# Kernel tuning notes

Hardware: AMD Instinct MI355X
Metric: run time of the kernel (lower is better)

## Reference

```python
import jax, jax.numpy as jnp
import numpy as np

MAX_DELTAS = 4  # number of concurrently loaded delta adapters


def _dequant(qw, qz, sc):
    """GPTQ-style 4-bit dequant with a single group (g_idx == 0).

    qw: [D, O, K//8] int32, 8 x 4-bit values packed along the input (K) dim.
    qz: [D, O//8, 1] int32, 8 x 4-bit zero points packed along the output dim.
    sc: [D, O, 1] float scales (one group).
    Returns dense delta weights [D, O, K].
    """
    shifts = jnp.arange(8, dtype=jnp.int32) * 4
    D, O, Kp = qw.shape
    w = ((qw[:, :, :, None] >> shifts) & 0xF).reshape(D, O, Kp * 8)   # [D,O,K]
    z = ((qz[:, :, 0][:, :, None] >> shifts) & 0xF).reshape(D, O)     # [D,O]
    return (w.astype(sc.dtype) - (z.astype(sc.dtype) + 1.0)[:, :, None]) * sc


def setup_inputs() -> dict:
    key = jax.random.key(0)
    ks = jax.random.split(key, 16)
    T, IN = 1024, 4096
    Q, KV = 4096, 1024  # 32 q-heads, 8 kv-heads, head_size 128
    OUT = Q + 2 * KV    # 6144
    D, PACK = MAX_DELTAS, 8
    IMAX = np.int32(2**31 - 1)
    return {
        "x": jax.random.normal(ks[0], (T, IN), dtype=jnp.float32),
        "w_base": jax.random.normal(ks[1], (OUT, IN), dtype=jnp.float32) * 0.02,
        "bias": jax.random.normal(ks[2], (OUT,), dtype=jnp.float32) * 0.02,
        "qweight_q": jax.random.randint(ks[3], (D, Q, IN // PACK), 0, IMAX, dtype=jnp.int32),
        "qweight_k": jax.random.randint(ks[4], (D, KV, IN // PACK), 0, IMAX, dtype=jnp.int32),
        "qweight_v": jax.random.randint(ks[5], (D, KV, IN // PACK), 0, IMAX, dtype=jnp.int32),
        "qzeros_q": jax.random.randint(ks[6], (D, Q // PACK, 1), 0, IMAX, dtype=jnp.int32),
        "qzeros_k": jax.random.randint(ks[7], (D, KV // PACK, 1), 0, IMAX, dtype=jnp.int32),
        "qzeros_v": jax.random.randint(ks[8], (D, KV // PACK, 1), 0, IMAX, dtype=jnp.int32),
        "scales_q": jax.random.uniform(ks[9], (D, Q, 1), dtype=jnp.float32) * 0.01,
        "scales_k": jax.random.uniform(ks[10], (D, KV, 1), dtype=jnp.float32) * 0.01,
        "scales_v": jax.random.uniform(ks[11], (D, KV, 1), dtype=jnp.float32) * 0.01,
        "indices": jax.random.randint(ks[12], (T,), 0, D, dtype=jnp.int32),
    }


def reference(x, w_base, bias, qweight_q, qweight_k, qweight_v,
              qzeros_q, qzeros_k, qzeros_v, scales_q, scales_k, scales_v,
              indices):
    # Base fused QKV projection.
    out = x @ w_base.T + bias  # [T, OUT]
    # Dequantize the three packed delta stacks and concatenate along out dim,
    # matching the (q, k, v) output_slices scatter of apply_delta.
    Wd = jnp.concatenate([
        _dequant(qweight_q, qzeros_q, scales_q),
        _dequant(qweight_k, qzeros_k, scales_k),
        _dequant(qweight_v, qzeros_v, scales_v),
    ], axis=1)  # [D, OUT, IN]
    # Per-token indexed delta matmul: token t uses adapter indices[t].
    for d in range(MAX_DELTAS):
        xm = jnp.where((indices == d)[:, None], x, 0.0)  # [T, IN]
        out = out + xm @ Wd[d].T
    return out
```

## Files before the change

### kernel.cpp

```cpp
#include <hip/hip_runtime.h>
#include <stdint.h>

#define T_TOK 1024
#define K_IN  4096
#define N_OUT 6144
#define N_Q   4096
#define N_KV  1024
#define N_D   4
#define KP    512

#define TM 128
#define TN 128
#define BK 64
#define NSTEPS (K_IN / BK)
#define PM_MAX 1536
#define MT (PM_MAX/TM)
#define NT (N_OUT/TN)
#define NBLK (NT * MT)

typedef __attribute__((ext_vector_type(8)))  short  short8;
typedef __attribute__((ext_vector_type(4)))  float  float4v;
typedef __attribute__((ext_vector_type(4)))  float  f32x4;
typedef __attribute__((ext_vector_type(4)))  uint   u32x4;

__device__ __forceinline__ ushort f2bf(float f) {
    uint32_t u = __float_as_uint(f);
    u = (u + 0x7FFFu + ((u >> 16) & 1u)) >> 16;
    return (ushort)u;
}
__device__ __forceinline__ uint pack2(ushort a, ushort b) {
    return (uint)a | ((uint)b << 16);
}

__device__ __forceinline__ short8 unpack_nib(uint q) {
    union { u32x4 u; short8 s; } r;
    uint t1 = q >> 8, t2 = q >> 16, t3 = q >> 24;
    r.u.x = ((q  & 0xFu) | ((q  & 0xF0u) << 12)) | 0x43004300u;
    r.u.y = ((t1 & 0xFu) | ((t1 & 0xF0u) << 12)) | 0x43004300u;
    r.u.z = ((t2 & 0xFu) | ((t2 & 0xF0u) << 12)) | 0x43004300u;
    r.u.w = ((t3 & 0xFu) | ((t3 & 0xF0u) << 12)) | 0x43004300u;
    return r.s;
}

__global__ void build_perm_kernel(const int* __restrict__ indices,
                                  int* __restrict__ perm,
                                  int* __restrict__ pofs) {
    int tid = threadIdx.x;
    for (int p = tid; p < PM_MAX; p += 256) perm[p] = -1;
    __syncthreads();
    if (tid >= 64) return;

    int cnt0 = 0, cnt1 = 0, cnt2 = 0, cnt3 = 0;
#pragma unroll
    for (int it = 0; it < T_TOK / 64; it++) {
        int d = indices[it * 64 + tid];
        cnt0 += __popcll(__ballot(d == 0));
        cnt1 += __popcll(__ballot(d == 1));
        cnt2 += __popcll(__ballot(d == 2));
        cnt3 += __popcll(__ballot(d == 3));
    }
    int cnt[4] = {cnt0, cnt1, cnt2, cnt3};
    int ps[5];
    int run = 0;
#pragma unroll
    for (int d = 0; d < N_D; d++) { ps[d] = run; run += ((cnt[d] + TM - 1) / TM) * TM; }
    ps[N_D] = run;
    if (tid == 0) {
#pragma unroll
        for (int d = 0; d <= N_D; d++) pofs[d] = ps[d];
    }
    unsigned long long ltmask = (tid == 63) ? 0x7FFFFFFFFFFFFFFFull
                                            : ((1ull << tid) - 1ull);
    int base[4] = {0, 0, 0, 0};
#pragma unroll
    for (int it = 0; it < T_TOK / 64; it++) {
        int d = indices[it * 64 + tid];
        unsigned long long m0 = __ballot(d == 0);
        unsigned long long m1 = __ballot(d == 1);
        unsigned long long m2 = __ballot(d == 2);
        unsigned long long m3 = __ballot(d == 3);
        unsigned long long md = (d == 0) ? m0 : (d == 1) ? m1 : (d == 2) ? m2 : m3;
        int rank = (int)__popcll(md & ltmask);
        int bse  = (d == 0) ? base[0] : (d == 1) ? base[1] : (d == 2) ? base[2] : base[3];
        int psd  = (d == 0) ? ps[0]   : (d == 1) ? ps[1]   : (d == 2) ? ps[2]   : ps[3];
        perm[psd + bse + rank] = it * 64 + tid;
        base[0] += __popcll(m0); base[1] += __popcll(m1);
        base[2] += __popcll(m2); base[3] += __popcll(m3);
    }
}

__global__ void wbconv_kernel(const float* __restrict__ w_base,
                              ushort* __restrict__ wb16) {
    int id = blockIdx.x * blockDim.x + threadIdx.x;
    const f32x4* src = (const f32x4*)(w_base + (size_t)id * 8);
    f32x4 a = __builtin_nontemporal_load(src);
    f32x4 b = __builtin_nontemporal_load(src + 1);
    u32x4 packv;
    packv.x = pack2(f2bf(a.x), f2bf(a.y));
    packv.y = pack2(f2bf(a.z), f2bf(a.w));
    packv.z = pack2(f2bf(b.x), f2bf(b.y));
    packv.w = pack2(f2bf(b.z), f2bf(b.w));
    *(u32x4*)(wb16 + (size_t)id * 8) = packv;
}

__global__ void repack_qw_kernel(const int* __restrict__ qw_q,
                                 const int* __restrict__ qw_k,
                                 const int* __restrict__ qw_v,
                                 uint* __restrict__ qp) {
    int b  = blockIdx.x;
    int s8 = b & 7;
    int r  = b >> 3;
    int w2 = r & 1; r >>= 1;
    int d  = r & 3;
    int bn = r >> 2;
    const int* qw; int r0, Osec;
    if (bn < 32)      { qw = qw_q; r0 = bn * 128;        Osec = N_Q;  }
    else if (bn < 40) { qw = qw_k; r0 = (bn - 32) * 128; Osec = N_KV; }
    else              { qw = qw_v; r0 = (bn - 40) * 128; Osec = N_KV; }

    __shared__ int lds[64 * 64];
    int tid = threadIdx.x;
#pragma unroll
    for (int k = 0; k < 4; k++) {
        int p   = k * 256 + tid;
        int row = p >> 4, c4 = p & 15;
        const int* src = qw + ((size_t)d * Osec + r0 + w2 * 64 + row) * KP + s8 * 64 + c4 * 4;
        *(u32x4*)&lds[row * 64 + c4 * 4] = *(const u32x4*)src;
    }
    __syncthreads();
    size_t obase = (size_t)b * 4096;
#pragma unroll
    for (int k = 0; k < 2; k++) {
        int p    = k * 256 + tid;
        int sl   = p >> 6, lane = p & 63;
        int quad = lane >> 4, l16 = lane & 15;
        uint pk[8];
#pragma unroll
        for (int e = 0; e < 8; e++) {
            int jj = e >> 1, h = e & 1;
            pk[e] = (uint)lds[(jj * 16 + l16) * 64 + sl * 8 + h * 4 + quad];
        }
        *(u32x4*)(qp + obase + (size_t)p * 8)     = *(u32x4*)&pk[0];
        *(u32x4*)(qp + obase + (size_t)p * 8 + 4) = *(u32x4*)&pk[4];
    }
}

__global__ void build_xp_kernel(const float* __restrict__ x,
                                const int* __restrict__ perm,
                                ushort* __restrict__ xp,
                                float* __restrict__ rs) {
    int pm = blockIdx.x;
    int half = blockIdx.y;
    int c0 = half * (K_IN / 2) + threadIdx.x * 8;
    int tok = perm[pm];
    ushort res[8];
    if (tok < 0) {
#pragma unroll
        for (int j = 0; j < 8; j++) res[j] = 0;
    } else {
        const f32x4* src = (const f32x4*)(x + (size_t)tok * K_IN + c0);
        f32x4 a = __builtin_nontemporal_load(src);
        f32x4 b = __builtin_nontemporal_load(src + 1);
        float v[8] = {a.x, a.y, a.z, a.w, b.x, b.y, b.z, b.w};
#pragma unroll
        for (int j = 0; j < 8; j++) res[j] = f2bf(v[j]);
    }
    u32x4 packv;
    packv.x = pack2(res[0], res[1]); packv.y = pack2(res[2], res[3]);
    packv.z = pack2(res[4], res[5]); packv.w = pack2(res[6], res[7]);
    *(u32x4*)(xp + (size_t)pm * K_IN + c0) = packv;

    float ssum = 0.f;
#pragma unroll
    for (int j = 0; j < 8; j++) ssum += __uint_as_float((uint)res[j] << 16);
#pragma unroll
    for (int off = 32; off > 0; off >>= 1) ssum += __shfl_xor(ssum, off);
    __shared__ float wsum[4];
    if ((threadIdx.x & 63) == 0) wsum[threadIdx.x >> 6] = ssum;
    __syncthreads();
    if (threadIdx.x == 0) rs[pm * 2 + half] = wsum[0] + wsum[1] + wsum[2] + wsum[3];
}

__global__ __launch_bounds__(256, 2) void gemm_kernel(
    const ushort* __restrict__ xp, const ushort* __restrict__ wb16,
    const uint* __restrict__ qp,
    const int* __restrict__ qz_q, const int* __restrict__ qz_k, const int* __restrict__ qz_v,
    const float* __restrict__ sc_q, const float* __restrict__ sc_k, const float* __restrict__ sc_v,
    const float* __restrict__ bias,
    const int* __restrict__ perm, const int* __restrict__ pofs,
    const float* __restrict__ rs,
    float* __restrict__ out) {

    __shared__ ushort As[2][TM * BK];
    __shared__ ushort Bs[2][TN * BK];

    int lin  = blockIdx.x;
    int low3 = lin & 7, rest = lin >> 3;
    int bm   = rest % MT, bq = rest / MT;
    int bn   = bq * 8 + low3;

    int m0 = bm * TM, n0 = bn * TN;
    int ptot = pofs[N_D];
    if (m0 >= ptot) return;
    int d = 0;
    while (d < N_D - 1 && m0 >= pofs[d + 1]) d++;

    int tid  = threadIdx.x;
    int lane = tid & 63;
    int wv   = tid >> 6;
    int wm   = (wv & 1) * 64;
    int wn   = (wv >> 1) * 64;
    int quad = lane >> 4;
    int l16  = lane & 15;
    int xa   = l16 & 7;

    const uint* qpw = qp + (((size_t)(bn * 4 + d) * 2 + (wv >> 1)) * 64 * 64 * 8)
                         + (size_t)lane * 8;

    const float4v zero4 = {0.f, 0.f, 0.f, 0.f};
    float4v acc_b[4][4], acc_d[4][4];
#pragma unroll
    for (int i = 0; i < 4; i++)
#pragma unroll
        for (int jj = 0; jj < 4; jj++) { acc_b[i][jj] = zero4; acc_d[i][jj] = zero4; }

    auto stage = [&](ushort* dstA, ushort* dstB, int k0) {
#pragma unroll
        for (int w = 0; w < 4; w++) {
            int p   = w * 256 + tid;
            int row = p >> 3;
            int ckl = (p & 7) ^ (row & 7);
            const ushort* ga = xp   + (size_t)(m0 + row) * K_IN + k0 + ckl * 8;
            const ushort* gb = wb16 + (size_t)(n0 + row) * K_IN + k0 + ckl * 8;
            int base = (w * 256 + (tid & ~63)) * 8;
            __builtin_amdgcn_global_load_lds((const __attribute__((address_space(1))) void*)ga,
                                             (__attribute__((address_space(3))) void*)(dstA + base), 16, 0, 0);
            __builtin_amdgcn_global_load_lds((const __attribute__((address_space(1))) void*)gb,
                                             (__attribute__((address_space(3))) void*)(dstB + base), 16, 0, 0);
        }
    };

    int buf = 0;
    stage(As[0], Bs[0], 0);
    uint q_cur[8];
    *(u32x4*)&q_cur[0] = *(const u32x4*)(qpw);
    *(u32x4*)&q_cur[4] = *(const u32x4*)(qpw + 4);
    __syncthreads();

    for (int s = 0; s < NSTEPS; s++) {
        uint q_nxt[8];
        if (s + 1 < NSTEPS) {
            stage(As[1 - buf], Bs[1 - buf], (s + 1) * BK);
            const uint* qn = qpw + (size_t)(s + 1) * 512;
            *(u32x4*)&q_nxt[0] = *(const u32x4*)(qn);
            *(u32x4*)&q_nxt[4] = *(const u32x4*)(qn + 4);
        }

        const ushort* Ab = As[buf];
        const ushort* Bb = Bs[buf];
#pragma unroll
        for (int kk = 0; kk < BK; kk += 32) {
            int h   = kk >> 5;
            int ckb = (kk >> 3) + quad;
            short8 a[4], b[4], bd[4];
#pragma unroll
            for (int i = 0; i < 4; i++)
                a[i] = *(const short8*)(Ab + (wm + i * 16 + l16) * BK + (ckb ^ xa) * 8);
#pragma unroll
            for (int jj = 0; jj < 4; jj++)
                b[jj] = *(const short8*)(Bb + (wn + jj * 16 + l16) * BK + (ckb ^ xa) * 8);
#pragma unroll
            for (int jj = 0; jj < 4; jj++)
                bd[jj] = unpack_nib(q_cur[jj * 2 + h]);
#pragma unroll
            for (int i = 0; i < 4; i++)
#pragma unroll
                for (int jj = 0; jj < 4; jj++) {
                    acc_b[i][jj] = __builtin_amdgcn_mfma_f32_16x16x32_bf16(a[i], b[jj],  acc_b[i][jj], 0, 0, 0);
                    acc_d[i][jj] = __builtin_amdgcn_mfma_f32_16x16x32_bf16(a[i], bd[jj], acc_d[i][jj], 0, 0, 0);
                }
        }
        __syncthreads();
#pragma unroll
        for (int e = 0; e < 8; e++) q_cur[e] = q_nxt[e];
        buf ^= 1;
    }

    const int* qz; const float* sc; int r0, Osec;
    if (n0 < N_Q)            { qz = qz_q; sc = sc_q; r0 = n0;                Osec = N_Q;  }
    else if (n0 < N_Q + N_KV){ qz = qz_k; sc = sc_k; r0 = n0 - N_Q;          Osec = N_KV; }
    else                     { qz = qz_v; sc = sc_v; r0 = n0 - (N_Q + N_KV); Osec = N_KV; }

    float s4[4], cc4[4], bv4[4];
#pragma unroll
    for (int jj = 0; jj < 4; jj++) {
        int rsec = r0 + wn + jj * 16 + l16;
        float sv = sc[(size_t)d * Osec + rsec];
        int   zq = qz[(size_t)d * (Osec >> 3) + (rsec >> 3)];
        int   z  = (zq >> ((rsec & 7) * 4)) & 0xF;
        s4[jj]  = sv;
        cc4[jj] = sv * (float)(129 + z);
        bv4[jj] = bias[n0 + wn + jj * 16 + l16];
    }
#pragma unroll
    for (int i = 0; i < 4; i++) {
        int toks[4]; float rsv[4];
#pragma unroll
        for (int r = 0; r < 4; r++) {
            int row = m0 + wm + i * 16 + quad * 4 + r;
            toks[r] = perm[row];
            rsv[r]  = rs[row * 2] + rs[row * 2 + 1];
        }
#pragma unroll
        for (int jj = 0; jj < 4; jj++) {
            int col = n0 + wn + jj * 16 + l16;
#pragma unroll
            for (int r = 0; r < 4; r++) {
                int tok = toks[r];
                if (tok >= 0) {
                    float v = bv4[jj] + acc_b[i][jj][r] + s4[jj] * acc_d[i][jj][r] - cc4[jj] * rsv[r];
                    out[(size_t)tok * N_OUT + col] = v;
                }
            }
        }
    }
}

extern "C" void kernel_launch(void* const* d_in, const int* in_sizes, int n_in,
                              void* d_out, int out_size, void* d_ws, size_t ws_size,
                              hipStream_t stream) {
    const float* x      = (const float*)d_in[0];
    const float* w_base = (const float*)d_in[1];
    const float* bias   = (const float*)d_in[2];
    const int*   qw_q   = (const int*)d_in[3];
    const int*   qw_k   = (const int*)d_in[4];
    const int*   qw_v   = (const int*)d_in[5];
    const int*   qz_q   = (const int*)d_in[6];
    const int*   qz_k   = (const int*)d_in[7];
    const int*   qz_v   = (const int*)d_in[8];
    const float* sc_q   = (const float*)d_in[9];
    const float* sc_k   = (const float*)d_in[10];
    const float* sc_v   = (const float*)d_in[11];
    const int*   indices= (const int*)d_in[12];
    float* out = (float*)d_out;

    char* ws = (char*)d_ws;
    ushort* wb16 = (ushort*)ws;
    size_t wb_bytes = (size_t)N_OUT * K_IN * 2;
    ushort* xp = (ushort*)(ws + wb_bytes);
    size_t xp_bytes = (size_t)PM_MAX * K_IN * 2;
    float* rsum = (float*)(ws + wb_bytes + xp_bytes);
    size_t rs_bytes = (size_t)PM_MAX * 2 * sizeof(float);
    int* perm = (int*)(ws + wb_bytes + xp_bytes + rs_bytes);
    int* pofs = perm + PM_MAX;
    uint* qp  = (uint*)(ws + wb_bytes + xp_bytes + rs_bytes + PM_MAX * 4 + 64);

    build_perm_kernel<<<1, 256, 0, stream>>>(indices, perm, pofs);
    wbconv_kernel<<<(N_OUT * K_IN / 8) / 256, 256, 0, stream>>>(w_base, wb16);
    repack_qw_kernel<<<48 * 4 * 2 * 8, 256, 0, stream>>>(qw_q, qw_k, qw_v, qp);
    build_xp_kernel<<<dim3(PM_MAX, 2), 256, 0, stream>>>(x, perm, xp, rsum);
    gemm_kernel<<<NBLK, 256, 0, stream>>>(xp, wb16, qp,
        qz_q, qz_k, qz_v, sc_q, sc_k, sc_v, bias,
        perm, pofs, rsum, out);
}
```

Baseline: 443.0 us.

## Halve GEMM M-tile to cut padding, merge prep kernels, parallelize permutation build

Shrinks the GEMM row tile from 128 to 64 so per-adapter padding drops (PM_MAX 1536 to 1280), reducing wasted MFMA work on padded rows, and raises launch bounds to three blocks per CU. The three preprocessing kernels (weight bf16 conversion, qweight repack, x gather) are fused into one launch partitioned by block index. The permutation builder is rewritten to use 1024 threads with a shared-memory prefix over wave counts instead of a serial single-wave loop. Smaller tiles lower arithmetic intensity per B-tile load, so B traffic rises.

```diff
diff --git a/kernel.cpp b/kernel.cpp
--- a/kernel.cpp
+++ b/kernel.cpp
@@ -9,14 +9,18 @@
 #define N_D   4
 #define KP    512
 
-#define TM 128
+#define TM 64
 #define TN 128
 #define BK 64
 #define NSTEPS (K_IN / BK)
-#define PM_MAX 1536
+#define PM_MAX 1280
 #define MT (PM_MAX/TM)
 #define NT (N_OUT/TN)
 #define NBLK (NT * MT)
+
+#define NB_WB ((N_OUT * K_IN / 8) / 256)
+#define NB_RP (48 * 4 * 2 * 8)
+#define NB_XP (PM_MAX * 2)
 
 typedef __attribute__((ext_vector_type(8)))  short  short8;
 typedef __attribute__((ext_vector_type(4)))  float  float4v;
@@ -45,143 +49,128 @@
 __global__ void build_perm_kernel(const int* __restrict__ indices,
                                   int* __restrict__ perm,
                                   int* __restrict__ pofs) {
+    __shared__ int cw[16][4];
+    __shared__ int pw[16][4];
+    __shared__ int ps[N_D + 1];
     int tid = threadIdx.x;
-    for (int p = tid; p < PM_MAX; p += 256) perm[p] = -1;
+    for (int p = tid; p < PM_MAX; p += 1024) perm[p] = -1;
+
+    int d = indices[tid];
+    unsigned long long m[4];
+    m[0] = __ballot(d == 0); m[1] = __ballot(d == 1);
+    m[2] = __ballot(d == 2); m[3] = __ballot(d == 3);
+    int lane = tid & 63, wv = tid >> 6;
+    if (lane < 4) cw[wv][lane] = (int)__popcll(m[lane]);
     __syncthreads();
-    if (tid >= 64) return;
-
-    int cnt0 = 0, cnt1 = 0, cnt2 = 0, cnt3 = 0;
-#pragma unroll
-    for (int it = 0; it < T_TOK / 64; it++) {
-        int d = indices[it * 64 + tid];
-        cnt0 += __popcll(__ballot(d == 0));
-        cnt1 += __popcll(__ballot(d == 1));
-        cnt2 += __popcll(__ballot(d == 2));
-        cnt3 += __popcll(__ballot(d == 3));
-    }
-    int cnt[4] = {cnt0, cnt1, cnt2, cnt3};
-    int ps[5];
-    int run = 0;
-#pragma unroll
-    for (int d = 0; d < N_D; d++) { ps[d] = run; run += ((cnt[d] + TM - 1) / TM) * TM; }
-    ps[N_D] = run;
     if (tid == 0) {
-#pragma unroll
-        for (int d = 0; d <= N_D; d++) pofs[d] = ps[d];
-    }
-    unsigned long long ltmask = (tid == 63) ? 0x7FFFFFFFFFFFFFFFull
-                                            : ((1ull << tid) - 1ull);
-    int base[4] = {0, 0, 0, 0};
-#pragma unroll
-    for (int it = 0; it < T_TOK / 64; it++) {
-        int d = indices[it * 64 + tid];
-        unsigned long long m0 = __ballot(d == 0);
-        unsigned long long m1 = __ballot(d == 1);
-        unsigned long long m2 = __ballot(d == 2);
-        unsigned long long m3 = __ballot(d == 3);
-        unsigned long long md = (d == 0) ? m0 : (d == 1) ? m1 : (d == 2) ? m2 : m3;
-        int rank = (int)__popcll(md & ltmask);
-        int bse  = (d == 0) ? base[0] : (d == 1) ? base[1] : (d == 2) ? base[2] : base[3];
-        int psd  = (d == 0) ? ps[0]   : (d == 1) ? ps[1]   : (d == 2) ? ps[2]   : ps[3];
-        perm[psd + bse + rank] = it * 64 + tid;
-        base[0] += __popcll(m0); base[1] += __popcll(m1);
-        base[2] += __popcll(m2); base[3] += __popcll(m3);
-    }
-}
-
-__global__ void wbconv_kernel(const float* __restrict__ w_base,
-                              ushort* __restrict__ wb16) {
-    int id = blockIdx.x * blockDim.x + threadIdx.x;
-    const f32x4* src = (const f32x4*)(w_base + (size_t)id * 8);
-    f32x4 a = __builtin_nontemporal_load(src);
-    f32x4 b = __builtin_nontemporal_load(src + 1);
-    u32x4 packv;
-    packv.x = pack2(f2bf(a.x), f2bf(a.y));
-    packv.y = pack2(f2bf(a.z), f2bf(a.w));
-    packv.z = pack2(f2bf(b.x), f2bf(b.y));
-    packv.w = pack2(f2bf(b.z), f2bf(b.w));
-    *(u32x4*)(wb16 + (size_t)id * 8) = packv;
-}
-
-__global__ void repack_qw_kernel(const int* __restrict__ qw_q,
-                                 const int* __restrict__ qw_k,
-                                 const int* __restrict__ qw_v,
-                                 uint* __restrict__ qp) {
-    int b  = blockIdx.x;
-    int s8 = b & 7;
-    int r  = b >> 3;
-    int w2 = r & 1; r >>= 1;
-    int d  = r & 3;
-    int bn = r >> 2;
-    const int* qw; int r0, Osec;
-    if (bn < 32)      { qw = qw_q; r0 = bn * 128;        Osec = N_Q;  }
-    else if (bn < 40) { qw = qw_k; r0 = (bn - 32) * 128; Osec = N_KV; }
-    else              { qw = qw_v; r0 = (bn - 40) * 128; Osec = N_KV; }
-
-    __shared__ int lds[64 * 64];
+        int tot[4] = {0, 0, 0, 0};
+        for (int w = 0; w < 16; w++)
+            for (int dd = 0; dd < 4; dd++) { pw[w][dd] = tot[dd]; tot[dd] += cw[w][dd]; }
+        int run = 0;
+        for (int dd = 0; dd < N_D; dd++) { ps[dd] = run; run += ((tot[dd] + TM - 1) / TM) * TM; }
+        ps[N_D] = run;
+        for (int dd = 0; dd <= N_D; dd++) pofs[dd] = ps[dd];
+    }
+    __syncthreads();
+    unsigned long long lt = (1ull << lane) - 1ull;
+    int rank = pw[wv][d] + (int)__popcll(m[d] & lt);
+    perm[ps[d] + rank] = tid;
+}
+
+__global__ void prep_kernel(const float* __restrict__ w_base, ushort* __restrict__ wb16,
+                            const int* __restrict__ qw_q, const int* __restrict__ qw_k,
+                            const int* __restrict__ qw_v, uint* __restrict__ qp,
+                            const float* __restrict__ x, const int* __restrict__ perm,
+                            ushort* __restrict__ xp, float* __restrict__ rs) {
+    __shared__ int slds[64 * 64];
     int tid = threadIdx.x;
-#pragma unroll
-    for (int k = 0; k < 4; k++) {
-        int p   = k * 256 + tid;
-        int row = p >> 4, c4 = p & 15;
-        const int* src = qw + ((size_t)d * Osec + r0 + w2 * 64 + row) * KP + s8 * 64 + c4 * 4;
-        *(u32x4*)&lds[row * 64 + c4 * 4] = *(const u32x4*)src;
-    }
-    __syncthreads();
-    size_t obase = (size_t)b * 4096;
-#pragma unroll
-    for (int k = 0; k < 2; k++) {
-        int p    = k * 256 + tid;
-        int sl   = p >> 6, lane = p & 63;
-        int quad = lane >> 4, l16 = lane & 15;
-        uint pk[8];
-#pragma unroll
-        for (int e = 0; e < 8; e++) {
-            int jj = e >> 1, h = e & 1;
-            pk[e] = (uint)lds[(jj * 16 + l16) * 64 + sl * 8 + h * 4 + quad];
-        }
-        *(u32x4*)(qp + obase + (size_t)p * 8)     = *(u32x4*)&pk[0];
-        *(u32x4*)(qp + obase + (size_t)p * 8 + 4) = *(u32x4*)&pk[4];
-    }
-}
-
-__global__ void build_xp_kernel(const float* __restrict__ x,
-                                const int* __restrict__ perm,
-                                ushort* __restrict__ xp,
-                                float* __restrict__ rs) {
-    int pm = blockIdx.x;
-    int half = blockIdx.y;
-    int c0 = half * (K_IN / 2) + threadIdx.x * 8;
-    int tok = perm[pm];
-    ushort res[8];
-    if (tok < 0) {
-#pragma unroll
-        for (int j = 0; j < 8; j++) res[j] = 0;
-    } else {
-        const f32x4* src = (const f32x4*)(x + (size_t)tok * K_IN + c0);
+    int b = blockIdx.x;
+
+    if (b < NB_WB) {
+        int id = b * 256 + tid;
+        const f32x4* src = (const f32x4*)(w_base + (size_t)id * 8);
         f32x4 a = __builtin_nontemporal_load(src);
-        f32x4 b = __builtin_nontemporal_load(src + 1);
-        float v[8] = {a.x, a.y, a.z, a.w, b.x, b.y, b.z, b.w};
-#pragma unroll
-        for (int j = 0; j < 8; j++) res[j] = f2bf(v[j]);
-    }
-    u32x4 packv;
-    packv.x = pack2(res[0], res[1]); packv.y = pack2(res[2], res[3]);
-    packv.z = pack2(res[4], res[5]); packv.w = pack2(res[6], res[7]);
-    *(u32x4*)(xp + (size_t)pm * K_IN + c0) = packv;
-
-    float ssum = 0.f;
-#pragma unroll
-    for (int j = 0; j < 8; j++) ssum += __uint_as_float((uint)res[j] << 16);
-#pragma unroll
-    for (int off = 32; off > 0; off >>= 1) ssum += __shfl_xor(ssum, off);
-    __shared__ float wsum[4];
-    if ((threadIdx.x & 63) == 0) wsum[threadIdx.x >> 6] = ssum;
-    __syncthreads();
-    if (threadIdx.x == 0) rs[pm * 2 + half] = wsum[0] + wsum[1] + wsum[2] + wsum[3];
-}
-
-__global__ __launch_bounds__(256, 2) void gemm_kernel(
+        f32x4 c = __builtin_nontemporal_load(src + 1);
+        u32x4 packv;
+        packv.x = pack2(f2bf(a.x), f2bf(a.y));
+        packv.y = pack2(f2bf(a.z), f2bf(a.w));
+        packv.z = pack2(f2bf(c.x), f2bf(c.y));
+        packv.w = pack2(f2bf(c.z), f2bf(c.w));
+        *(u32x4*)(wb16 + (size_t)id * 8) = packv;
+        return;
+    }
+    b -= NB_WB;
+    if (b < NB_RP) {
+        int s8 = b & 7;
+        int r  = b >> 3;
+        int w2 = r & 1; r >>= 1;
+        int d  = r & 3;
+        int bn = r >> 2;
+        const int* qw; int r0, Osec;
+        if (bn < 32)      { qw = qw_q; r0 = bn * 128;        Osec = N_Q;  }
+        else if (bn < 40) { qw = qw_k; r0 = (bn - 32) * 128; Osec = N_KV; }
+        else              { qw = qw_v; r0 = (bn - 40) * 128; Osec = N_KV; }
+#pragma unroll
+        for (int k = 0; k < 4; k++) {
+            int p   = k * 256 + tid;
+            int row = p >> 4, c4 = p & 15;
+            const int* src = qw + ((size_t)d * Osec + r0 + w2 * 64 + row) * KP + s8 * 64 + c4 * 4;
+            *(u32x4*)&slds[row * 64 + c4 * 4] = *(const u32x4*)src;
+        }
+        __syncthreads();
+        size_t obase = (size_t)b * 4096;
+#pragma unroll
+        for (int k = 0; k < 2; k++) {
+            int p    = k * 256 + tid;
+            int sl   = p >> 6, lane = p & 63;
+            int quad = lane >> 4, l16 = lane & 15;
+            uint pk[8];
+#pragma unroll
+            for (int e = 0; e < 8; e++) {
+                int jj = e >> 1, h = e & 1;
+                pk[e] = (uint)slds[(jj * 16 + l16) * 64 + sl * 8 + h * 4 + quad];
+            }
+            *(u32x4*)(qp + obase + (size_t)p * 8)     = *(u32x4*)&pk[0];
+            *(u32x4*)(qp + obase + (size_t)p * 8 + 4) = *(u32x4*)&pk[4];
+        }
+        return;
+    }
+    b -= NB_RP;
+    {
+        int pm = b >> 1;
+        int half = b & 1;
+        int c0 = half * (K_IN / 2) + tid * 8;
+        int tok = perm[pm];
+        ushort res[8];
+        if (tok < 0) {
+#pragma unroll
+            for (int j = 0; j < 8; j++) res[j] = 0;
+        } else {
+            const f32x4* src = (const f32x4*)(x + (size_t)tok * K_IN + c0);
+            f32x4 a = __builtin_nontemporal_load(src);
+            f32x4 c = __builtin_nontemporal_load(src + 1);
+            float v[8] = {a.x, a.y, a.z, a.w, c.x, c.y, c.z, c.w};
+#pragma unroll
+            for (int j = 0; j < 8; j++) res[j] = f2bf(v[j]);
+        }
+        u32x4 packv;
+        packv.x = pack2(res[0], res[1]); packv.y = pack2(res[2], res[3]);
+        packv.z = pack2(res[4], res[5]); packv.w = pack2(res[6], res[7]);
+        *(u32x4*)(xp + (size_t)pm * K_IN + c0) = packv;
+
+        float ssum = 0.f;
+#pragma unroll
+        for (int j = 0; j < 8; j++) ssum += __uint_as_float((uint)res[j] << 16);
+#pragma unroll
+        for (int off = 32; off > 0; off >>= 1) ssum += __shfl_xor(ssum, off);
+        float* wsum = (float*)slds;
+        if ((tid & 63) == 0) wsum[tid >> 6] = ssum;
+        __syncthreads();
+        if (tid == 0) rs[pm * 2 + half] = wsum[0] + wsum[1] + wsum[2] + wsum[3];
+    }
+}
+
+__global__ __launch_bounds__(256, 3) void gemm_kernel(
     const ushort* __restrict__ xp, const ushort* __restrict__ wb16,
     const uint* __restrict__ qp,
     const int* __restrict__ qz_q, const int* __restrict__ qz_k, const int* __restrict__ qz_v,
@@ -208,7 +197,7 @@
     int tid  = threadIdx.x;
     int lane = tid & 63;
     int wv   = tid >> 6;
-    int wm   = (wv & 1) * 64;
+    int wm   = (wv & 1) * 32;
     int wn   = (wv >> 1) * 64;
     int quad = lane >> 4;
     int l16  = lane & 15;
@@ -218,23 +207,30 @@
                          + (size_t)lane * 8;
 
     const float4v zero4 = {0.f, 0.f, 0.f, 0.f};
-    float4v acc_b[4][4], acc_d[4][4];
-#pragma unroll
-    for (int i = 0; i < 4; i++)
+    float4v acc_b[2][4], acc_d[2][4];
+#pragma unroll
+    for (int i = 0; i < 2; i++)
 #pragma unroll
         for (int jj = 0; jj < 4; jj++) { acc_b[i][jj] = zero4; acc_d[i][jj] = zero4; }
 
     auto stage = [&](ushort* dstA, ushort* dstB, int k0) {
+#pragma unroll
+        for (int w = 0; w < 2; w++) {
+            int p   = w * 256 + tid;
+            int row = p >> 3;
+            int ckl = (p & 7) ^ (row & 7);
+            const ushort* ga = xp + (size_t)(m0 + row) * K_IN + k0 + ckl * 8;
+            int base = (w * 256 + (tid & ~63)) * 8;
+            __builtin_amdgcn_global_load_lds((const __attribute__((address_space(1))) void*)ga,
+                                             (__attribute__((address_space(3))) void*)(dstA + base), 16, 0, 0);
+        }
 #pragma unroll
         for (int w = 0; w < 4; w++) {
             int p   = w * 256 + tid;
             int row = p >> 3;
             int ckl = (p & 7) ^ (row & 7);
-            const ushort* ga = xp   + (size_t)(m0 + row) * K_IN + k0 + ckl * 8;
             const ushort* gb = wb16 + (size_t)(n0 + row) * K_IN + k0 + ckl * 8;
             int base = (w * 256 + (tid & ~63)) * 8;
-            __builtin_amdgcn_global_load_lds((const __attribute__((address_space(1))) void*)ga,
-                                             (__attribute__((address_space(3))) void*)(dstA + base), 16, 0, 0);
             __builtin_amdgcn_global_load_lds((const __attribute__((address_space(1))) void*)gb,
                                              (__attribute__((address_space(3))) void*)(dstB + base), 16, 0, 0);
         }
@@ -262,9 +258,9 @@
         for (int kk = 0; kk < BK; kk += 32) {
             int h   = kk >> 5;
             int ckb = (kk >> 3) + quad;
-            short8 a[4], b[4], bd[4];
-#pragma unroll
-            for (int i = 0; i < 4; i++)
+            short8 a[2], b[4], bd[4];
+#pragma unroll
+            for (int i = 0; i < 2; i++)
                 a[i] = *(const short8*)(Ab + (wm + i * 16 + l16) * BK + (ckb ^ xa) * 8);
 #pragma unroll
             for (int jj = 0; jj < 4; jj++)
@@ -273,7 +269,7 @@
             for (int jj = 0; jj < 4; jj++)
                 bd[jj] = unpack_nib(q_cur[jj * 2 + h]);
 #pragma unroll
-            for (int i = 0; i < 4; i++)
+            for (int i = 0; i < 2; i++)
 #pragma unroll
                 for (int jj = 0; jj < 4; jj++) {
                     acc_b[i][jj] = __builtin_amdgcn_mfma_f32_16x16x32_bf16(a[i], b[jj],  acc_b[i][jj], 0, 0, 0);
@@ -303,7 +299,7 @@
         bv4[jj] = bias[n0 + wn + jj * 16 + l16];
     }
 #pragma unroll
-    for (int i = 0; i < 4; i++) {
+    for (int i = 0; i < 2; i++) {
         int toks[4]; float rsv[4];
 #pragma unroll
         for (int r = 0; r < 4; r++) {
@@ -355,10 +351,9 @@
     int* pofs = perm + PM_MAX;
     uint* qp  = (uint*)(ws + wb_bytes + xp_bytes + rs_bytes + PM_MAX * 4 + 64);
 
-    build_perm_kernel<<<1, 256, 0, stream>>>(indices, perm, pofs);
-    wbconv_kernel<<<(N_OUT * K_IN / 8) / 256, 256, 0, stream>>>(w_base, wb16);
-    repack_qw_kernel<<<48 * 4 * 2 * 8, 256, 0, stream>>>(qw_q, qw_k, qw_v, qp);
-    build_xp_kernel<<<dim3(PM_MAX, 2), 256, 0, stream>>>(x, perm, xp, rsum);
+    build_perm_kernel<<<1, 1024, 0, stream>>>(indices, perm, pofs);
+    prep_kernel<<<NB_WB + NB_RP + NB_XP, 256, 0, stream>>>(
+        w_base, wb16, qw_q, qw_k, qw_v, qp, x, perm, xp, rsum);
     gemm_kernel<<<NBLK, 256, 0, stream>>>(xp, wb16, qp,
         qz_q, qz_k, qz_v, sc_q, sc_k, sc_v, bias,
         perm, pofs, rsum, out);
```

Result: faster. 413.4 us (-6.7%).
